# Kernel optimization log

Hardware: AMD Instinct MI355X
Metric: run time of the kernel (lower is better)

The kernel has to match this reference:

```python
import jax, jax.numpy as jnp
import numpy as np

N_NODES = 10000
N_EDGES = 640000
IN_C = 128
HID = 256
OUT_C = 256


def _linear_params(key, fan_in, fan_out):
    k1, k2 = jax.random.split(key)
    bound = 1.0 / np.sqrt(fan_in)
    W = jax.random.uniform(k1, (fan_in, fan_out), jnp.float32, -bound, bound)
    b = jax.random.uniform(k2, (fan_out,), jnp.float32, -bound, bound)
    return W, b


def setup_inputs() -> dict:
    key = jax.random.key(0)
    ks = jax.random.split(key, 8)
    x = jax.random.normal(ks[0], (N_NODES, IN_C), jnp.float32)
    edge_index = jax.random.randint(ks[1], (2, N_EDGES), 0, N_NODES, jnp.int32)
    W0a, b0a = _linear_params(ks[2], IN_C, HID)
    W0b, b0b = _linear_params(ks[3], HID, HID)
    W1a, b1a = _linear_params(ks[4], HID, HID)
    W1b, b1b = _linear_params(ks[5], HID, HID)
    W2a, b2a = _linear_params(ks[6], HID, OUT_C)
    W2b, b2b = _linear_params(ks[7], OUT_C, OUT_C)
    return {"x": x, "edge_index": edge_index,
            "W0a": W0a, "b0a": b0a, "W0b": W0b, "b0b": b0b,
            "W1a": W1a, "b1a": b1a, "W1b": W1b, "b1b": b1b,
            "W2a": W2a, "b2a": b2a, "W2b": W2b, "b2b": b2b}


def _gin_conv(x, src, dst, Wa, ba, Wb, bb):
    # sum-aggregate neighbor features: agg[i] = sum_{(j->i) in E} x[j]
    agg = jax.ops.segment_sum(x[src], dst, num_segments=N_NODES)
    h = x + agg  # eps = 0 (PyG GINConv default): (1+eps)*x + agg
    h = jnp.maximum(h @ Wa + ba, 0.0) @ Wb + bb  # Linear-ReLU-Linear MLP
    return h


def reference(x, edge_index, W0a, b0a, W0b, b0b, W1a, b1a, W1b, b1b, W2a, b2a, W2b, b2b):
    src, dst = edge_index[0], edge_index[1]
    h = _gin_conv(x, src, dst, W0a, b0a, W0b, b0b)
    h = jnp.maximum(h, 0.0)  # ReLU; dropout is identity in eval mode
    h = _gin_conv(h, src, dst, W1a, b1a, W1b, b1b)
    h = jnp.maximum(h, 0.0)
    h = _gin_conv(h, src, dst, W2a, b2a, W2b, b2b)
    return h
```

## Files before the change

kernel.cpp:

```cpp
#include <hip/hip_runtime.h>

#define N_NODES 10000
#define N_EDGES 640000
#define ELL_W   128
#define NB      157
#define BCAP    4600
#define LCAP    80
#define CHUNK   2500

typedef short short8 __attribute__((ext_vector_type(8)));
typedef float f32x4 __attribute__((ext_vector_type(4)));

__device__ inline float bf2f(unsigned short u) {
    return __uint_as_float(((unsigned)u) << 16);
}
__device__ inline unsigned short f2bf(float f) {
    unsigned u = __float_as_uint(f);
    u += 0x7fffu + ((u >> 16) & 1u);
    return (unsigned short)(u >> 16);
}

__global__ __launch_bounds__(256) void zero_cursor(int* __restrict__ g) {
    if (threadIdx.x < NB) g[threadIdx.x] = 0;
}

__global__ __launch_bounds__(256) void bin_edges(const int* __restrict__ src,
                                                 const int* __restrict__ dst,
                                                 int* __restrict__ gCursor,
                                                 unsigned* __restrict__ gBucket) {
    __shared__ unsigned bins[NB][LCAP];
    __shared__ int cnt[NB];
    __shared__ int base[NB];
    int t = threadIdx.x;
    for (int i = t; i < NB; i += 256) cnt[i] = 0;
    __syncthreads();

    int e0 = blockIdx.x * CHUNK;
    int e1 = min(e0 + CHUNK, N_EDGES);
    for (int e = e0 + t; e < e1; e += 256) {
        int d = dst[e];
        int b = d >> 6;
        unsigned pk = ((unsigned)src[e] << 6) | (unsigned)(d & 63);
        int p = atomicAdd(&cnt[b], 1);
        if (p < LCAP) bins[b][p] = pk;
    }
    __syncthreads();
    for (int i = t; i < NB; i += 256) {
        int c = min(cnt[i], LCAP);
        cnt[i] = c;
        base[i] = atomicAdd(&gCursor[i], c);
    }
    __syncthreads();
    int wave = t >> 6, lane = t & 63;
    for (int b = wave; b < NB; b += 4) {
        int ba = base[b];
        int n = min(cnt[b], max(0, BCAP - ba));
        for (int i = lane; i < n; i += 64)
            gBucket[(size_t)b * BCAP + ba + i] = bins[b][i];
    }
}

__global__ __launch_bounds__(256) void build_ell(const unsigned* __restrict__ gBucket,
                                                 const int* __restrict__ gCursor,
                                                 unsigned short* __restrict__ ell,
                                                 int* __restrict__ deg) {
    __shared__ unsigned short rows[64 * ELL_W];
    __shared__ int ldeg[64];
    int b = blockIdx.x;
    int t = threadIdx.x;
    for (int i = t; i < 64; i += 256) ldeg[i] = 0;
    __syncthreads();

    int n = min(gCursor[b], BCAP);
    const unsigned* bk = gBucket + (size_t)b * BCAP;
    for (int i = t; i < n; i += 256) {
        unsigned pk = bk[i];
        int local = pk & 63;
        int s = pk >> 6;
        int p = atomicAdd(&ldeg[local], 1);
        if (p < ELL_W) rows[local * ELL_W + p] = (unsigned short)s;
    }
    __syncthreads();

    int node0 = b * 64;
    int nNodes = min(64, N_NODES - node0);
    if (nNodes <= 0) return;
    for (int i = t; i < nNodes; i += 256)
        deg[node0 + i] = min(ldeg[i], ELL_W);
    int totalVec = nNodes * (ELL_W / 8);
    short8* dstv = (short8*)(ell + (size_t)node0 * ELL_W);
    const short8* srcv = (const short8*)rows;
    for (int i = t; i < totalVec; i += 256) dstv[i] = srcv[i];
}

__global__ __launch_bounds__(256) void cvt_x_kernel(const float4* __restrict__ x,
                                                    ushort4* __restrict__ xb, int n4) {
    int i = blockIdx.x * 256 + threadIdx.x;
    if (i >= n4) return;
    float4 v = x[i];
    ushort4 o;
    o.x = f2bf(v.x); o.y = f2bf(v.y); o.z = f2bf(v.z); o.w = f2bf(v.w);
    xb[i] = o;
}

struct WList {
    const float* src[6];
    unsigned short* dst[6];
    int K[6];
    int off[7];
};

__global__ __launch_bounds__(256) void cvt_w_kernel(WList wl, int total) {
    int idx = blockIdx.x * 256 + threadIdx.x;
    if (idx >= total) return;
    int w = 0;
    while (idx >= wl.off[w + 1]) ++w;
    int r = idx - wl.off[w];
    int k = r >> 8;
    int n = r & 255;
    wl.dst[w][(size_t)n * wl.K[w] + k] = f2bf(wl.src[w][r]);
}

template <int U2STRIDE>
__global__ __launch_bounds__(256) void gather_ell(const unsigned* __restrict__ x,
                                                  const unsigned short* __restrict__ ell,
                                                  const int* __restrict__ deg,
                                                  unsigned* __restrict__ out) {
    int wid = (blockIdx.x * 256 + threadIdx.x) >> 6;
    int lane = threadIdx.x & 63;
    if (wid >= N_NODES) return;
    int off = blockIdx.y * 64 + lane;

    unsigned v = x[(size_t)wid * U2STRIDE + off];
    float a0 = bf2f((unsigned short)(v & 0xffff));
    float a1 = bf2f((unsigned short)(v >> 16));

    int dg = min(deg[wid], ELL_W);
    const unsigned short* row = ell + (size_t)wid * ELL_W;

    int j = 0;
    for (; j + 8 <= dg; j += 8) {
        ushort4 sA = *(const ushort4*)(row + j);
        ushort4 sB = *(const ushort4*)(row + j + 4);
        unsigned v0 = x[(size_t)sA.x * U2STRIDE + off];
        unsigned v1 = x[(size_t)sA.y * U2STRIDE + off];
        unsigned v2 = x[(size_t)sA.z * U2STRIDE + off];
        unsigned v3 = x[(size_t)sA.w * U2STRIDE + off];
        unsigned v4 = x[(size_t)sB.x * U2STRIDE + off];
        unsigned v5 = x[(size_t)sB.y * U2STRIDE + off];
        unsigned v6 = x[(size_t)sB.z * U2STRIDE + off];
        unsigned v7 = x[(size_t)sB.w * U2STRIDE + off];
        a0 += (bf2f((unsigned short)(v0 & 0xffff)) + bf2f((unsigned short)(v1 & 0xffff))) +
              (bf2f((unsigned short)(v2 & 0xffff)) + bf2f((unsigned short)(v3 & 0xffff))) +
              (bf2f((unsigned short)(v4 & 0xffff)) + bf2f((unsigned short)(v5 & 0xffff))) +
              (bf2f((unsigned short)(v6 & 0xffff)) + bf2f((unsigned short)(v7 & 0xffff)));
        a1 += (bf2f((unsigned short)(v0 >> 16)) + bf2f((unsigned short)(v1 >> 16))) +
              (bf2f((unsigned short)(v2 >> 16)) + bf2f((unsigned short)(v3 >> 16))) +
              (bf2f((unsigned short)(v4 >> 16)) + bf2f((unsigned short)(v5 >> 16))) +
              (bf2f((unsigned short)(v6 >> 16)) + bf2f((unsigned short)(v7 >> 16)));
    }
    for (; j < dg; ++j) {
        unsigned vv = x[(size_t)row[j] * U2STRIDE + off];
        a0 += bf2f((unsigned short)(vv & 0xffff));
        a1 += bf2f((unsigned short)(vv >> 16));
    }
    unsigned o = (unsigned)f2bf(a0) | ((unsigned)f2bf(a1) << 16);
    out[(size_t)wid * U2STRIDE + off] = o;
}

template <int KSTEPS, bool RELU, bool F32OUT>
__global__ __launch_bounds__(64) void gemm_mfma(const unsigned short* __restrict__ A,
                                                const unsigned short* __restrict__ Wt,
                                                const float* __restrict__ bias,
                                                void* __restrict__ Cout) {
    constexpr int K = KSTEPS * 32;
    int bid = blockIdx.x;
    int rowtile = bid >> 2;
    int nq = bid & 3;
    int r0 = rowtile * 32;
    int lane = threadIdx.x;
    int lrow = lane & 15;
    int lkg = lane >> 4;

    const short8* Ap0 = (const short8*)(A + (size_t)(r0 + lrow) * K + lkg * 8);
    const short8* Ap1 = (const short8*)(A + (size_t)(r0 + 16 + lrow) * K + lkg * 8);
    int n0 = nq * 64;
    const short8* Bp = (const short8*)(Wt + (size_t)(n0 + lrow) * K + lkg * 8);
    f32x4 acc[2][4] = {};

#pragma unroll
    for (int ks = 0; ks < KSTEPS; ++ks) {
        short8 a0 = Ap0[ks * 4];
        short8 a1 = Ap1[ks * 4];
        short8 b0 = Bp[ks * 4 + 0 * 2 * K];
        short8 b1 = Bp[ks * 4 + 1 * 2 * K];
        short8 b2 = Bp[ks * 4 + 2 * 2 * K];
        short8 b3 = Bp[ks * 4 + 3 * 2 * K];
        acc[0][0] = __builtin_amdgcn_mfma_f32_16x16x32_bf16(a0, b0, acc[0][0], 0, 0, 0);
        acc[0][1] = __builtin_amdgcn_mfma_f32_16x16x32_bf16(a0, b1, acc[0][1], 0, 0, 0);
        acc[0][2] = __builtin_amdgcn_mfma_f32_16x16x32_bf16(a0, b2, acc[0][2], 0, 0, 0);
        acc[0][3] = __builtin_amdgcn_mfma_f32_16x16x32_bf16(a0, b3, acc[0][3], 0, 0, 0);
        acc[1][0] = __builtin_amdgcn_mfma_f32_16x16x32_bf16(a1, b0, acc[1][0], 0, 0, 0);
        acc[1][1] = __builtin_amdgcn_mfma_f32_16x16x32_bf16(a1, b1, acc[1][1], 0, 0, 0);
        acc[1][2] = __builtin_amdgcn_mfma_f32_16x16x32_bf16(a1, b2, acc[1][2], 0, 0, 0);
        acc[1][3] = __builtin_amdgcn_mfma_f32_16x16x32_bf16(a1, b3, acc[1][3], 0, 0, 0);
    }

#pragma unroll
    for (int rg = 0; rg < 2; ++rg) {
        int orow = r0 + rg * 16 + lkg * 4;
#pragma unroll
        for (int nt = 0; nt < 4; ++nt) {
            int c = n0 + nt * 16 + lrow;
            float bv = bias[c];
#pragma unroll
            for (int r = 0; r < 4; ++r) {
                int grow = orow + r;
                if (grow >= N_NODES) continue;
                float v = acc[rg][nt][r] + bv;
                if (RELU) v = fmaxf(v, 0.f);
                if (F32OUT)
                    ((float*)Cout)[(size_t)grow * 256 + c] = v;
                else
                    ((unsigned short*)Cout)[(size_t)grow * 256 + c] = f2bf(v);
            }
        }
    }
}

extern "C" void kernel_launch(void* const* d_in, const int* in_sizes, int n_in,
                              void* d_out, int out_size, void* d_ws, size_t ws_size,
                              hipStream_t stream) {
    const float* x   = (const float*)d_in[0];
    const int*   ei  = (const int*)d_in[1];
    const int*   src = ei;
    const int*   dst = ei + N_EDGES;
    const float* W0a = (const float*)d_in[2];
    const float* b0a = (const float*)d_in[3];
    const float* W0b = (const float*)d_in[4];
    const float* b0b = (const float*)d_in[5];
    const float* W1a = (const float*)d_in[6];
    const float* b1a = (const float*)d_in[7];
    const float* W1b = (const float*)d_in[8];
    const float* b1b = (const float*)d_in[9];
    const float* W2a = (const float*)d_in[10];
    const float* b2a = (const float*)d_in[11];
    const float* W2b = (const float*)d_in[12];
    const float* b2b = (const float*)d_in[13];

    char* ws = (char*)d_ws;
    size_t off = 0;
    auto alloc = [&](size_t bytes) {
        void* p = ws + off;
        off += (bytes + 255) & ~(size_t)255;
        return p;
    };
    unsigned short* xb    = (unsigned short*)alloc((size_t)N_NODES * 128 * 2);
    unsigned short* B0    = (unsigned short*)alloc((size_t)N_NODES * 256 * 2);
    unsigned short* B1    = (unsigned short*)alloc((size_t)N_NODES * 256 * 2);
    unsigned short* B2    = (unsigned short*)alloc((size_t)N_NODES * 256 * 2);
    unsigned short* Wt0a  = (unsigned short*)alloc(256 * 128 * 2);
    unsigned short* Wt0b  = (unsigned short*)alloc(256 * 256 * 2);
    unsigned short* Wt1a  = (unsigned short*)alloc(256 * 256 * 2);
    unsigned short* Wt1b  = (unsigned short*)alloc(256 * 256 * 2);
    unsigned short* Wt2a  = (unsigned short*)alloc(256 * 256 * 2);
    unsigned short* Wt2b  = (unsigned short*)alloc(256 * 256 * 2);
    int*            deg   = (int*)alloc(N_NODES * 4);
    unsigned short* ell   = (unsigned short*)alloc((size_t)N_NODES * ELL_W * 2);
    int*            gCur  = (int*)alloc(NB * 4);
    unsigned*       gBkt  = (unsigned*)alloc((size_t)NB * BCAP * 4);

    dim3 gatherGrid1((N_NODES + 3) / 4, 1);
    dim3 gatherGrid2((N_NODES + 3) / 4, 2);
    int gemmBlocks = ((N_NODES + 31) / 32) * 4;

    zero_cursor<<<1, 256, 0, stream>>>(gCur);
    bin_edges<<<(N_EDGES + CHUNK - 1) / CHUNK, 256, 0, stream>>>(src, dst, gCur, gBkt);
    build_ell<<<NB, 256, 0, stream>>>(gBkt, gCur, ell, deg);

    cvt_x_kernel<<<(N_NODES * 128 / 4 + 255) / 256, 256, 0, stream>>>(
        (const float4*)x, (ushort4*)xb, N_NODES * 128 / 4);
    WList wl;
    wl.src[0] = W0a; wl.dst[0] = Wt0a; wl.K[0] = 128;
    wl.src[1] = W0b; wl.dst[1] = Wt0b; wl.K[1] = 256;
    wl.src[2] = W1a; wl.dst[2] = Wt1a; wl.K[2] = 256;
    wl.src[3] = W1b; wl.dst[3] = Wt1b; wl.K[3] = 256;
    wl.src[4] = W2a; wl.dst[4] = Wt2a; wl.K[4] = 256;
    wl.src[5] = W2b; wl.dst[5] = Wt2b; wl.K[5] = 256;
    int total = 0;
    for (int i = 0; i < 6; ++i) { wl.off[i] = total; total += wl.K[i] * 256; }
    wl.off[6] = total;
    cvt_w_kernel<<<(total + 255) / 256, 256, 0, stream>>>(wl, total);

    gather_ell<64><<<gatherGrid1, 256, 0, stream>>>((const unsigned*)xb, ell, deg, (unsigned*)B0);
    gemm_mfma<4, true, false><<<gemmBlocks, 64, 0, stream>>>(B0, Wt0a, b0a, B1);
    gemm_mfma<8, true, false><<<gemmBlocks, 64, 0, stream>>>(B1, Wt0b, b0b, B2);
    gather_ell<128><<<gatherGrid2, 256, 0, stream>>>((const unsigned*)B2, ell, deg, (unsigned*)B0);
    gemm_mfma<8, true, false><<<gemmBlocks, 64, 0, stream>>>(B0, Wt1a, b1a, B1);
    gemm_mfma<8, true, false><<<gemmBlocks, 64, 0, stream>>>(B1, Wt1b, b1b, B2);
    gather_ell<128><<<gatherGrid2, 256, 0, stream>>>((const unsigned*)B2, ell, deg, (unsigned*)B0);
    gemm_mfma<8, true, false><<<gemmBlocks, 64, 0, stream>>>(B0, Wt2a, b2a, B1);
    gemm_mfma<8, false, true><<<gemmBlocks, 64, 0, stream>>>(B1, Wt2b, b2b, d_out);
}
```

Before: 179.2 us.

## Stage GEMM weight tiles in LDS across four waves; widen gather unroll

The GEMM now runs 256-thread blocks covering 128 rows. Each block loads its 64-column weight slice into padded shared memory once, and the four waves reuse it from LDS instead of each wave re-reading the weights from global memory. The ELL gather loop is unrolled to 16 neighbours per iteration using short8 index loads, with a 4-wide remainder loop, to keep more independent loads in flight. The trade-off is a block-wide sync, up to about 33KB of LDS per block, and fewer GEMM blocks, which may cut occupancy and parallelism.

```diff
diff --git a/kernel.cpp b/kernel.cpp
--- a/kernel.cpp
+++ b/kernel.cpp
@@ -139,25 +139,32 @@
     const unsigned short* row = ell + (size_t)wid * ELL_W;
 
     int j = 0;
-    for (; j + 8 <= dg; j += 8) {
+    for (; j + 16 <= dg; j += 16) {
+        short8 iA = *(const short8*)(row + j);
+        short8 iB = *(const short8*)(row + j + 8);
+        unsigned vv[16];
+#pragma unroll
+        for (int q = 0; q < 8; ++q)
+            vv[q] = x[(size_t)(unsigned short)iA[q] * U2STRIDE + off];
+#pragma unroll
+        for (int q = 0; q < 8; ++q)
+            vv[8 + q] = x[(size_t)(unsigned short)iB[q] * U2STRIDE + off];
+#pragma unroll
+        for (int q = 0; q < 16; ++q) {
+            a0 += bf2f((unsigned short)(vv[q] & 0xffff));
+            a1 += bf2f((unsigned short)(vv[q] >> 16));
+        }
+    }
+    for (; j + 4 <= dg; j += 4) {
         ushort4 sA = *(const ushort4*)(row + j);
-        ushort4 sB = *(const ushort4*)(row + j + 4);
         unsigned v0 = x[(size_t)sA.x * U2STRIDE + off];
         unsigned v1 = x[(size_t)sA.y * U2STRIDE + off];
         unsigned v2 = x[(size_t)sA.z * U2STRIDE + off];
         unsigned v3 = x[(size_t)sA.w * U2STRIDE + off];
-        unsigned v4 = x[(size_t)sB.x * U2STRIDE + off];
-        unsigned v5 = x[(size_t)sB.y * U2STRIDE + off];
-        unsigned v6 = x[(size_t)sB.z * U2STRIDE + off];
-        unsigned v7 = x[(size_t)sB.w * U2STRIDE + off];
         a0 += (bf2f((unsigned short)(v0 & 0xffff)) + bf2f((unsigned short)(v1 & 0xffff))) +
-              (bf2f((unsigned short)(v2 & 0xffff)) + bf2f((unsigned short)(v3 & 0xffff))) +
-              (bf2f((unsigned short)(v4 & 0xffff)) + bf2f((unsigned short)(v5 & 0xffff))) +
-              (bf2f((unsigned short)(v6 & 0xffff)) + bf2f((unsigned short)(v7 & 0xffff)));
+              (bf2f((unsigned short)(v2 & 0xffff)) + bf2f((unsigned short)(v3 & 0xffff)));
         a1 += (bf2f((unsigned short)(v0 >> 16)) + bf2f((unsigned short)(v1 >> 16))) +
-              (bf2f((unsigned short)(v2 >> 16)) + bf2f((unsigned short)(v3 >> 16))) +
-              (bf2f((unsigned short)(v4 >> 16)) + bf2f((unsigned short)(v5 >> 16))) +
-              (bf2f((unsigned short)(v6 >> 16)) + bf2f((unsigned short)(v7 >> 16)));
+              (bf2f((unsigned short)(v2 >> 16)) + bf2f((unsigned short)(v3 >> 16)));
     }
     for (; j < dg; ++j) {
         unsigned vv = x[(size_t)row[j] * U2STRIDE + off];
@@ -169,33 +176,50 @@
 }
 
 template <int KSTEPS, bool RELU, bool F32OUT>
-__global__ __launch_bounds__(64) void gemm_mfma(const unsigned short* __restrict__ A,
-                                                const unsigned short* __restrict__ Wt,
-                                                const float* __restrict__ bias,
-                                                void* __restrict__ Cout) {
+__global__ __launch_bounds__(256) void gemm_mfma(const unsigned short* __restrict__ A,
+                                                 const unsigned short* __restrict__ Wt,
+                                                 const float* __restrict__ bias,
+                                                 void* __restrict__ Cout) {
     constexpr int K = KSTEPS * 32;
+    constexpr int LP = K + 8;
+    __shared__ unsigned short Bs[64 * LP];
+
     int bid = blockIdx.x;
-    int rowtile = bid >> 2;
+    int rowblk = bid >> 2;
     int nq = bid & 3;
-    int r0 = rowtile * 32;
-    int lane = threadIdx.x;
+    int r0 = rowblk * 128;
+    int n0 = nq * 64;
+    int tid = threadIdx.x;
+
+    {
+        constexpr int V = 64 * (K / 8);
+        const short8* srcv = (const short8*)(Wt + (size_t)n0 * K);
+        for (int i = tid; i < V; i += 256) {
+            int r = i / (K / 8);
+            int c = i % (K / 8);
+            *(short8*)&Bs[r * LP + c * 8] = srcv[i];
+        }
+    }
+    __syncthreads();
+
+    int wave = tid >> 6, lane = tid & 63;
     int lrow = lane & 15;
     int lkg = lane >> 4;
-
-    const short8* Ap0 = (const short8*)(A + (size_t)(r0 + lrow) * K + lkg * 8);
-    const short8* Ap1 = (const short8*)(A + (size_t)(r0 + 16 + lrow) * K + lkg * 8);
-    int n0 = nq * 64;
-    const short8* Bp = (const short8*)(Wt + (size_t)(n0 + lrow) * K + lkg * 8);
+    int wr0 = r0 + wave * 32;
+    if (wr0 >= N_NODES) return;
+
+    const short8* Ap0 = (const short8*)(A + (size_t)(wr0 + lrow) * K + lkg * 8);
+    const short8* Ap1 = (const short8*)(A + (size_t)(wr0 + 16 + lrow) * K + lkg * 8);
     f32x4 acc[2][4] = {};
 
 #pragma unroll
     for (int ks = 0; ks < KSTEPS; ++ks) {
         short8 a0 = Ap0[ks * 4];
         short8 a1 = Ap1[ks * 4];
-        short8 b0 = Bp[ks * 4 + 0 * 2 * K];
-        short8 b1 = Bp[ks * 4 + 1 * 2 * K];
-        short8 b2 = Bp[ks * 4 + 2 * 2 * K];
-        short8 b3 = Bp[ks * 4 + 3 * 2 * K];
+        short8 b0 = *(const short8*)&Bs[(0 * 16 + lrow) * LP + ks * 32 + lkg * 8];
+        short8 b1 = *(const short8*)&Bs[(1 * 16 + lrow) * LP + ks * 32 + lkg * 8];
+        short8 b2 = *(const short8*)&Bs[(2 * 16 + lrow) * LP + ks * 32 + lkg * 8];
+        short8 b3 = *(const short8*)&Bs[(3 * 16 + lrow) * LP + ks * 32 + lkg * 8];
         acc[0][0] = __builtin_amdgcn_mfma_f32_16x16x32_bf16(a0, b0, acc[0][0], 0, 0, 0);
         acc[0][1] = __builtin_amdgcn_mfma_f32_16x16x32_bf16(a0, b1, acc[0][1], 0, 0, 0);
         acc[0][2] = __builtin_amdgcn_mfma_f32_16x16x32_bf16(a0, b2, acc[0][2], 0, 0, 0);
@@ -208,7 +232,7 @@
 
 #pragma unroll
     for (int rg = 0; rg < 2; ++rg) {
-        int orow = r0 + rg * 16 + lkg * 4;
+        int orow = wr0 + rg * 16 + lkg * 4;
 #pragma unroll
         for (int nt = 0; nt < 4; ++nt) {
             int c = n0 + nt * 16 + lrow;
@@ -272,7 +296,7 @@
 
     dim3 gatherGrid1((N_NODES + 3) / 4, 1);
     dim3 gatherGrid2((N_NODES + 3) / 4, 2);
-    int gemmBlocks = ((N_NODES + 31) / 32) * 4;
+    int gemmBlocks = ((N_NODES + 127) / 128) * 4;
 
     zero_cursor<<<1, 256, 0, stream>>>(gCur);
     bin_edges<<<(N_EDGES + CHUNK - 1) / CHUNK, 256, 0, stream>>>(src, dst, gCur, gBkt);
@@ -293,12 +317,12 @@
     cvt_w_kernel<<<(total + 255) / 256, 256, 0, stream>>>(wl, total);
 
     gather_ell<64><<<gatherGrid1, 256, 0, stream>>>((const unsigned*)xb, ell, deg, (unsigned*)B0);
-    gemm_mfma<4, true, false><<<gemmBlocks, 64, 0, stream>>>(B0, Wt0a, b0a, B1);
-    gemm_mfma<8, true, false><<<gemmBlocks, 64, 0, stream>>>(B1, Wt0b, b0b, B2);
+    gemm_mfma<4, true, false><<<gemmBlocks, 256, 0, stream>>>(B0, Wt0a, b0a, B1);
+    gemm_mfma<8, true, false><<<gemmBlocks, 256, 0, stream>>>(B1, Wt0b, b0b, B2);
     gather_ell<128><<<gatherGrid2, 256, 0, stream>>>((const unsigned*)B2, ell, deg, (unsigned*)B0);
-    gemm_mfma<8, true, false><<<gemmBlocks, 64, 0, stream>>>(B0, Wt1a, b1a, B1);
-    gemm_mfma<8, true, false><<<gemmBlocks, 64, 0, stream>>>(B1, Wt1b, b1b, B2);
+    gemm_mfma<8, true, false><<<gemmBlocks, 256, 0, stream>>>(B0, Wt1a, b1a, B1);
+    gemm_mfma<8, true, false><<<gemmBlocks, 256, 0, stream>>>(B1, Wt1b, b1b, B2);
     gather_ell<128><<<gatherGrid2, 256, 0, stream>>>((const unsigned*)B2, ell, deg, (unsigned*)B0);
-    gemm_mfma<8, true, false><<<gemmBlocks, 64, 0, stream>>>(B0, Wt2a, b2a, B1);
-    gemm_mfma<8, false, true><<<gemmBlocks, 64, 0, stream>>>(B1, Wt2b, b2b, d_out);
-}
+    gemm_mfma<8, true, false><<<gemmBlocks, 256, 0, stream>>>(B0, Wt2a, b2a, B1);
+    gemm_mfma<8, false, true><<<gemmBlocks, 256, 0, stream>>>(B1, Wt2b, b2b, d_out);
+}
```

New measurement: 163.1 us. -9.0%, faster.
